# Optimization experiments

Measured on AMD Instinct MI355X. Metric: run time of the kernel, lower is better.

Reference implementation:

```python
import jax, jax.numpy as jnp
import numpy as np

B, S, D, H = 2, 2048, 1024, 16
HD = D // H  # head_dim = 64


def setup_inputs() -> dict:
    key = jax.random.key(0)
    ks = jax.random.split(key, 6)
    sc = 0.02
    return {
        "x": jax.random.normal(ks[0], (B, S, D), dtype=jnp.float32),
        "W_query": jax.random.normal(ks[1], (D, D), dtype=jnp.float32) * sc,
        "W_key": jax.random.normal(ks[2], (D, D), dtype=jnp.float32) * sc,
        "W_value": jax.random.normal(ks[3], (D, D), dtype=jnp.float32) * sc,
        "W_out": jax.random.normal(ks[4], (D, D), dtype=jnp.float32) * sc,
        "b_out": jnp.zeros((D,), dtype=jnp.float32),
    }


def reference(x, W_query, W_key, W_value, W_out, b_out):
    b, s, _ = x.shape
    # torch nn.Linear: y = x @ W.T ; split into heads [b, h, s, hd]
    def proj(W):
        return (x @ W.T).reshape(b, s, H, HD).transpose(0, 2, 1, 3)

    q, k, v = proj(W_query), proj(W_key), proj(W_value)
    scores = jnp.einsum("bhqd,bhkd->bhqk", q, k)  # [b, h, s, s]
    causal = jnp.tril(jnp.ones((s, s), dtype=bool))  # True = keep
    scores = jnp.where(causal, scores, -jnp.inf)
    weights = jax.nn.softmax(scores / np.sqrt(HD).astype(np.float32), axis=-1)
    # dropout p=0.0 -> identity
    ctx = jnp.einsum("bhqk,bhkd->bhqd", weights, v)
    ctx = ctx.transpose(0, 2, 1, 3).reshape(b, s, D)
    return ctx @ W_out.T + b_out
```

## Files before the change

kernel.cpp:

```cpp
#include <hip/hip_runtime.h>
#include <stdint.h>

#define B_  2
#define S_  2048
#define D_  1024
#define H_  16
#define HD_ 64
#define M_  (B_*S_)

typedef __attribute__((ext_vector_type(8)))  short bf16x8;
typedef __attribute__((ext_vector_type(4)))  float f32x4;
typedef __attribute__((ext_vector_type(16))) float f32x16;
typedef __attribute__((ext_vector_type(4)))  unsigned int u32x4;


__device__ __forceinline__ unsigned short f2bf(float f) {
    unsigned int u = __float_as_uint(f);
    unsigned int r = (u + 0x7fffu + ((u >> 16) & 1u)) >> 16;
    return (unsigned short)r;
}

__device__ __forceinline__ unsigned int cvt_pk_bf16(float lo, float hi) {
    unsigned int r;
    asm("v_cvt_pk_bf16_f32 %0, %1, %2" : "=v"(r) : "v"(lo), "v"(hi));
    return r;
}

__device__ __forceinline__ void gload_lds16(const void* g, void* l) {
    __builtin_amdgcn_global_load_lds(
        (const __attribute__((address_space(1))) unsigned int*)g,
        (__attribute__((address_space(3))) unsigned int*)l,
        16, 0, 0);
}


__global__ __launch_bounds__(256) void cast_all(
    const float* __restrict__ x,
    const float* __restrict__ wq, const float* __restrict__ wk,
    const float* __restrict__ wv, const float* __restrict__ wo,
    unsigned short* __restrict__ dst)
{
    int b = blockIdx.x;
    const float* src;
    size_t soff, doff;
    float sc = 1.0f;
    if (b < 2048) {
        src = x; soff = (size_t)b * 2048; doff = soff;
    } else {
        int r  = (b - 2048) >> 9;
        int lb = (b - 2048) & 511;
        src = (r == 0) ? wq : (r == 1) ? wk : (r == 2) ? wv : wo;
        if (r <= 1) sc = 0.4246609093670877f;
        soff = (size_t)lb * 2048;
        doff = (size_t)4194304 + (size_t)r * 1048576 + soff;
    }
    int idx = threadIdx.x * 8;
    float4 a = *reinterpret_cast<const float4*>(src + soff + idx);
    float4 c = *reinterpret_cast<const float4*>(src + soff + idx + 4);
    unsigned short t[8];
    t[0]=f2bf(a.x*sc); t[1]=f2bf(a.y*sc); t[2]=f2bf(a.z*sc); t[3]=f2bf(a.w*sc);
    t[4]=f2bf(c.x*sc); t[5]=f2bf(c.y*sc); t[6]=f2bf(c.z*sc); t[7]=f2bf(c.w*sc);
    *reinterpret_cast<uint4*>(dst + doff + idx) = *reinterpret_cast<const uint4*>(t);
}


template <bool BIAS, typename CT>
__global__ __launch_bounds__(256) void gemm_bt(
    const unsigned short* __restrict__ A,
    const unsigned short* __restrict__ Bm,
    CT* __restrict__ C,
    const float* __restrict__ bias,
    int M, int N, int K)
{
    constexpr int BK = 32;
    __shared__ unsigned short As[128 * BK];
    __shared__ unsigned short Bs[128 * BK];

    const int tid  = threadIdx.x;
    const int lane = tid & 63;
    const int wid  = tid >> 6;
    const int wr = wid >> 1, wc = wid & 1;
    const int l15 = lane & 15, lhi = lane >> 4;
    const int tm = blockIdx.y * 128, tn = blockIdx.x * 128;

    f32x4 acc[4][4] = {};

    const int srow = (lane >> 2);
    const int scol = (lane & 3) * 8;

    for (int k0 = 0; k0 < K; k0 += BK) {
        __syncthreads();
        #pragma unroll
        for (int i = 0; i < 2; ++i) {
            int chunk = wid * 2 + i;
            int row = chunk * 16 + srow;
            gload_lds16(A  + (size_t)(tm + row) * K + k0 + scol, (void*)(As + chunk * 512));
            gload_lds16(Bm + (size_t)(tn + row) * K + k0 + scol, (void*)(Bs + chunk * 512));
        }
        __syncthreads();

        bf16x8 af[4], bfr[4];
        #pragma unroll
        for (int i = 0; i < 4; ++i)
            af[i] = *reinterpret_cast<const bf16x8*>(As + (wr * 64 + i * 16 + l15) * BK + lhi * 8);
        #pragma unroll
        for (int j = 0; j < 4; ++j)
            bfr[j] = *reinterpret_cast<const bf16x8*>(Bs + (wc * 64 + j * 16 + l15) * BK + lhi * 8);
        #pragma unroll
        for (int i = 0; i < 4; ++i)
            #pragma unroll
            for (int j = 0; j < 4; ++j)
                acc[i][j] = __builtin_amdgcn_mfma_f32_16x16x32_bf16(af[i], bfr[j], acc[i][j], 0, 0, 0);
    }

    #pragma unroll
    for (int i = 0; i < 4; ++i) {
        #pragma unroll
        for (int j = 0; j < 4; ++j) {
            int col = tn + wc * 64 + j * 16 + l15;
            float bv = BIAS ? bias[col] : 0.0f;
            #pragma unroll
            for (int r = 0; r < 4; ++r) {
                int row = tm + wr * 64 + i * 16 + lhi * 4 + r;
                float v = acc[i][j][r] + bv;
                if constexpr (sizeof(CT) == 2) {
                    ((unsigned short*)C)[(size_t)row * N + col] = f2bf(v);
                } else {
                    ((float*)C)[(size_t)row * N + col] = v;
                }
            }
        }
    }
}


__global__ __launch_bounds__(256) void gemm_qkv(
    const unsigned short* __restrict__ A,
    const unsigned short* __restrict__ Bm,
    unsigned short* __restrict__ Cqk,
    unsigned short* __restrict__ Vt)
{
    constexpr int BK = 32, K = 1024;
    __shared__ unsigned short As[128 * BK];
    __shared__ unsigned short Bs[128 * BK];

    const int tid  = threadIdx.x;
    const int lane = tid & 63;
    const int wid  = tid >> 6;
    const int wr = wid >> 1, wc = wid & 1;
    const int l15 = lane & 15, lhi = lane >> 4;
    const int tm = blockIdx.y * 128, tn = blockIdx.x * 128;

    f32x4 acc[4][4] = {};

    const int srow = (lane >> 2);
    const int scol = (lane & 3) * 8;

    for (int k0 = 0; k0 < K; k0 += BK) {
        __syncthreads();
        #pragma unroll
        for (int i = 0; i < 2; ++i) {
            int chunk = wid * 2 + i;
            int row = chunk * 16 + srow;
            gload_lds16(A  + (size_t)(tm + row) * K + k0 + scol, (void*)(As + chunk * 512));
            gload_lds16(Bm + (size_t)(tn + row) * K + k0 + scol, (void*)(Bs + chunk * 512));
        }
        __syncthreads();

        bf16x8 af[4], bfr[4];
        #pragma unroll
        for (int i = 0; i < 4; ++i)
            af[i] = *reinterpret_cast<const bf16x8*>(As + (wr * 64 + i * 16 + l15) * BK + lhi * 8);
        #pragma unroll
        for (int j = 0; j < 4; ++j)
            bfr[j] = *reinterpret_cast<const bf16x8*>(Bs + (wc * 64 + j * 16 + l15) * BK + lhi * 8);
        #pragma unroll
        for (int i = 0; i < 4; ++i)
            #pragma unroll
            for (int j = 0; j < 4; ++j)
                acc[i][j] = __builtin_amdgcn_mfma_f32_16x16x32_bf16(af[i], bfr[j], acc[i][j], 0, 0, 0);
    }

    const bool isV = (tn >= 2048);
    #pragma unroll
    for (int i = 0; i < 4; ++i) {
        #pragma unroll
        for (int j = 0; j < 4; ++j) {
            int col = tn + wc * 64 + j * 16 + l15;
            int row0 = tm + wr * 64 + i * 16 + lhi * 4;
            if (!isV) {
                #pragma unroll
                for (int r = 0; r < 4; ++r)
                    Cqk[(size_t)(row0 + r) * 2048 + col] = f2bf(acc[i][j][r]);
            } else {
                unsigned short t[4];
                #pragma unroll
                for (int r = 0; r < 4; ++r) t[r] = f2bf(acc[i][j][r]);
                *reinterpret_cast<uint2*>(Vt + (size_t)(col - 2048) * M_ + row0) =
                    *reinterpret_cast<const uint2*>(t);
            }
        }
    }
}


__global__ __launch_bounds__(256, 4) void attn_kernel(
    const unsigned short* __restrict__ QK,
    const unsigned short* __restrict__ VT,
    unsigned short* __restrict__ Ctx)
{
    __shared__ unsigned short Ks[4][32 * 64];
    __shared__ unsigned short Vs[4][64 * 32];

    const int tid  = threadIdx.x;
    const int lane = tid & 63;
    const int wid  = tid >> 6;
    const int l31  = lane & 31;
    const int hi   = lane >> 5;

    const int lin  = blockIdx.x;
    const int idx  = lin >> 3;
    const int bh   = (lin & 7) + 8 * (idx & 3);
    const int qb   = 63 - (idx >> 2);
    const int b = bh >> 4, h = bh & 15;
    const size_t baseRow = (size_t)b * S_;
    const int qw = qb * 32;
    const int q  = qw + l31;

    bf16x8 qf[4];
    #pragma unroll
    for (int s = 0; s < 4; ++s)
        qf[s] = *reinterpret_cast<const bf16x8*>(
            QK + (baseRow + q) * 2048 + h * HD_ + s * 16 + hi * 8);

    float l = 0.0f;
    f32x16 oacc[2] = {};

    const int nkt = qb + 1;

    const int kr  = lane >> 3;
    const int ks  = lane & 7;
    const int vr  = lane >> 2;
    const int vsl = lane & 3;

#define STAGE_K(kt_) do {                                                      \
    int k0_ = (kt_) * 32;                                                      \
    _Pragma("unroll")                                                          \
    for (int i_ = 0; i_ < 4; ++i_) {                                           \
        int krow_ = i_ * 8 + kr;                                               \
        int ksc_  = (ks ^ kr) * 8;                                             \
        gload_lds16(QK + (baseRow + k0_ + krow_) * 2048 + D_ + h * HD_ + ksc_, \
                    (void*)(&Ks[wid][i_ * 512]));                              \
    } } while (0)
#define STAGE_V(kt_) do {                                                      \
    int k0_ = (kt_) * 32;                                                      \
    _Pragma("unroll")                                                          \
    for (int i_ = 0; i_ < 4; ++i_) {                                           \
        int vrow_ = i_ * 16 + vr;                                              \
        int vsc_  = (vsl ^ ((vrow_ >> 1) & 3)) * 8;                            \
        gload_lds16(VT + (size_t)(h * HD_ + vrow_) * M_ + baseRow + k0_ + vsc_,\
                    (void*)(&Vs[wid][i_ * 512]));                              \
    } } while (0)

    if (wid < nkt) {
        STAGE_K(wid);
        STAGE_V(wid);
        for (int kt = wid; kt < nkt; kt += 4) {
            const bool more = (kt + 4 < nkt);

            asm volatile("s_waitcnt vmcnt(4)" ::: "memory");
            __builtin_amdgcn_sched_barrier(0);

            const unsigned short* Kc = &Ks[wid][0];

            f32x16 sc = {};
            #pragma unroll
            for (int s = 0; s < 4; ++s) {
                int sl = (2 * s + hi) ^ (l31 & 7);
                bf16x8 kf = *reinterpret_cast<const bf16x8*>(Kc + l31 * 64 + sl * 8);
                sc = __builtin_amdgcn_mfma_f32_32x32x16_bf16(kf, qf[s], sc, 0, 0, 0);
            }

            asm volatile("s_waitcnt lgkmcnt(0)" ::: "memory");
            __builtin_amdgcn_sched_barrier(0);
            if (more) STAGE_K(kt + 4);

            if (kt == qb) {
                #pragma unroll
                for (int r = 0; r < 16; ++r) {
                    int kl = kt * 32 + (r & 3) + 8 * (r >> 2) + 4 * hi;
                    if (kl > q) sc[r] = -INFINITY;
                }
            }

            unsigned int g0, g1, g2, g3, g4, g5, g6, g7;
            float ps = 0.0f;
            {
                float e0, e1, e2, e3;
                e0=exp2f(sc[0]);  e1=exp2f(sc[1]);  e2=exp2f(sc[2]);  e3=exp2f(sc[3]);
                ps += (e0+e1)+(e2+e3); g0 = cvt_pk_bf16(e0,e1); g1 = cvt_pk_bf16(e2,e3);
                e0=exp2f(sc[4]);  e1=exp2f(sc[5]);  e2=exp2f(sc[6]);  e3=exp2f(sc[7]);
                ps += (e0+e1)+(e2+e3); g2 = cvt_pk_bf16(e0,e1); g3 = cvt_pk_bf16(e2,e3);
                e0=exp2f(sc[8]);  e1=exp2f(sc[9]);  e2=exp2f(sc[10]); e3=exp2f(sc[11]);
                ps += (e0+e1)+(e2+e3); g4 = cvt_pk_bf16(e0,e1); g5 = cvt_pk_bf16(e2,e3);
                e0=exp2f(sc[12]); e1=exp2f(sc[13]); e2=exp2f(sc[14]); e3=exp2f(sc[15]);
                ps += (e0+e1)+(e2+e3); g6 = cvt_pk_bf16(e0,e1); g7 = cvt_pk_bf16(e2,e3);
            }
            l += ps;

            asm("v_permlane32_swap_b32 %0, %1" : "+v"(g0), "+v"(g2));
            asm("v_permlane32_swap_b32 %0, %1" : "+v"(g1), "+v"(g3));
            asm("v_permlane32_swap_b32 %0, %1" : "+v"(g4), "+v"(g6));
            asm("v_permlane32_swap_b32 %0, %1" : "+v"(g5), "+v"(g7));
            bf16x8 pa0 = __builtin_bit_cast(bf16x8, (u32x4){g0, g1, g2, g3});
            bf16x8 pa1 = __builtin_bit_cast(bf16x8, (u32x4){g4, g5, g6, g7});

            if (more) asm volatile("s_waitcnt vmcnt(4)" ::: "memory");
            else      asm volatile("s_waitcnt vmcnt(0)" ::: "memory");
            __builtin_amdgcn_sched_barrier(0);

            const unsigned short* Vc = &Vs[wid][0];
            bf16x8 vf[2][2];
            #pragma unroll
            for (int dt = 0; dt < 2; ++dt)
                #pragma unroll
                for (int s = 0; s < 2; ++s) {
                    int d = dt * 32 + l31;
                    int sl = (2 * s + hi) ^ ((d >> 1) & 3);
                    vf[dt][s] = *reinterpret_cast<const bf16x8*>(Vc + d * 32 + sl * 8);
                }

            asm volatile("s_waitcnt lgkmcnt(0)" ::: "memory");
            __builtin_amdgcn_sched_barrier(0);
            if (more) STAGE_V(kt + 4);

            __builtin_amdgcn_s_setprio(1);
            #pragma unroll
            for (int dt = 0; dt < 2; ++dt) {
                oacc[dt] = __builtin_amdgcn_mfma_f32_32x32x16_bf16(pa0, vf[dt][0], oacc[dt], 0, 0, 0);
                oacc[dt] = __builtin_amdgcn_mfma_f32_32x32x16_bf16(pa1, vf[dt][1], oacc[dt], 0, 0, 0);
            }
            __builtin_amdgcn_s_setprio(0);
        }
    }
#undef STAGE_K
#undef STAGE_V

    float* Olw = (float*)&Ks[wid][0];
    float* Lpw = (float*)&Vs[wid][0];
    float lc = l + __shfl_xor(l, 32, 64);
    if (hi == 0) Lpw[l31] = lc;

    const int cq = tid >> 3;
    const int cd = (tid & 7) * 4;
    float inv = 0.0f;
    #pragma unroll
    for (int ph = 0; ph < 2; ++ph) {
        __syncthreads();
        #pragma unroll
        for (int r = 0; r < 16; ++r) {
            int qr = (r & 3) + 8 * (r >> 2) + 4 * hi;
            Olw[qr * 32 + l31] = oacc[ph][r];
        }
        __syncthreads();
        float s0 = 0, s1 = 0, s2 = 0, s3 = 0, lt = 0;
        #pragma unroll
        for (int w = 0; w < 4; ++w) {
            const float* O = (const float*)&Ks[w][0];
            f32x4 a = *reinterpret_cast<const f32x4*>(O + cq * 32 + cd);
            s0 += a[0]; s1 += a[1]; s2 += a[2]; s3 += a[3];
            if (ph == 0) lt += ((const float*)&Vs[w][0])[cq];
        }
        if (ph == 0) inv = 1.0f / lt;
        unsigned short o[4];
        o[0] = f2bf(s0 * inv); o[1] = f2bf(s1 * inv);
        o[2] = f2bf(s2 * inv); o[3] = f2bf(s3 * inv);
        *reinterpret_cast<uint2*>(
            Ctx + (baseRow + qw + cq) * D_ + h * HD_ + ph * 32 + cd) =
            *reinterpret_cast<const uint2*>(o);
    }
}


extern "C" void kernel_launch(void* const* d_in, const int* in_sizes, int n_in,
                              void* d_out, int out_size, void* d_ws, size_t ws_size,
                              hipStream_t stream) {
    const float* x  = (const float*)d_in[0];
    const float* wq = (const float*)d_in[1];
    const float* wk = (const float*)d_in[2];
    const float* wv = (const float*)d_in[3];
    const float* wo = (const float*)d_in[4];
    const float* bo = (const float*)d_in[5];

    unsigned short* ws = (unsigned short*)d_ws;
    unsigned short* xb  = ws;
    unsigned short* wqb = xb  + 4194304;
    unsigned short* wob = wqb + 3145728;
    unsigned short* QKb = wob + 1048576;
    unsigned short* VT  = QKb + 8388608;
    unsigned short* Cx  = VT  + 4194304;

    cast_all<<<4096, 256, 0, stream>>>(x, wq, wk, wv, wo, xb);

    gemm_qkv<<<dim3(24, 32), 256, 0, stream>>>(xb, wqb, QKb, VT);

    attn_kernel<<<2048, 256, 0, stream>>>(QKb, VT, Cx);

    gemm_bt<true, float><<<dim3(8, 32), 256, 0, stream>>>(
        Cx, wob, (float*)d_out, bo, M_, D_, D_);
}
```

Before: 109.1 us.

## Pair causal query tiles per attention block and narrow output GEMM tiles

The attention kernel now gives each block two query tiles, a short one (pidx) and a long one (63-pidx). Each pair of waves splits that tile's key range across two waves instead of four, so per-block causal work is balanced and the grid shrinks from 2048 to 1024 blocks. The reduction epilogue combines only the two waves that belong to the same query tile and writes 16-byte stores. The output projection becomes a dedicated 128x64-tile GEMM with a 512-block grid, replacing the 128x128 generic one that used only 256 blocks. This fills more CUs, at the cost of less reuse per block and longer serial key loops per wave.

```diff
diff --git a/kernel.cpp b/kernel.cpp
--- a/kernel.cpp
+++ b/kernel.cpp
@@ -64,76 +64,6 @@
 }
 
 
-template <bool BIAS, typename CT>
-__global__ __launch_bounds__(256) void gemm_bt(
-    const unsigned short* __restrict__ A,
-    const unsigned short* __restrict__ Bm,
-    CT* __restrict__ C,
-    const float* __restrict__ bias,
-    int M, int N, int K)
-{
-    constexpr int BK = 32;
-    __shared__ unsigned short As[128 * BK];
-    __shared__ unsigned short Bs[128 * BK];
-
-    const int tid  = threadIdx.x;
-    const int lane = tid & 63;
-    const int wid  = tid >> 6;
-    const int wr = wid >> 1, wc = wid & 1;
-    const int l15 = lane & 15, lhi = lane >> 4;
-    const int tm = blockIdx.y * 128, tn = blockIdx.x * 128;
-
-    f32x4 acc[4][4] = {};
-
-    const int srow = (lane >> 2);
-    const int scol = (lane & 3) * 8;
-
-    for (int k0 = 0; k0 < K; k0 += BK) {
-        __syncthreads();
-        #pragma unroll
-        for (int i = 0; i < 2; ++i) {
-            int chunk = wid * 2 + i;
-            int row = chunk * 16 + srow;
-            gload_lds16(A  + (size_t)(tm + row) * K + k0 + scol, (void*)(As + chunk * 512));
-            gload_lds16(Bm + (size_t)(tn + row) * K + k0 + scol, (void*)(Bs + chunk * 512));
-        }
-        __syncthreads();
-
-        bf16x8 af[4], bfr[4];
-        #pragma unroll
-        for (int i = 0; i < 4; ++i)
-            af[i] = *reinterpret_cast<const bf16x8*>(As + (wr * 64 + i * 16 + l15) * BK + lhi * 8);
-        #pragma unroll
-        for (int j = 0; j < 4; ++j)
-            bfr[j] = *reinterpret_cast<const bf16x8*>(Bs + (wc * 64 + j * 16 + l15) * BK + lhi * 8);
-        #pragma unroll
-        for (int i = 0; i < 4; ++i)
-            #pragma unroll
-            for (int j = 0; j < 4; ++j)
-                acc[i][j] = __builtin_amdgcn_mfma_f32_16x16x32_bf16(af[i], bfr[j], acc[i][j], 0, 0, 0);
-    }
-
-    #pragma unroll
-    for (int i = 0; i < 4; ++i) {
-        #pragma unroll
-        for (int j = 0; j < 4; ++j) {
-            int col = tn + wc * 64 + j * 16 + l15;
-            float bv = BIAS ? bias[col] : 0.0f;
-            #pragma unroll
-            for (int r = 0; r < 4; ++r) {
-                int row = tm + wr * 64 + i * 16 + lhi * 4 + r;
-                float v = acc[i][j][r] + bv;
-                if constexpr (sizeof(CT) == 2) {
-                    ((unsigned short*)C)[(size_t)row * N + col] = f2bf(v);
-                } else {
-                    ((float*)C)[(size_t)row * N + col] = v;
-                }
-            }
-        }
-    }
-}
-
-
 __global__ __launch_bounds__(256) void gemm_qkv(
     const unsigned short* __restrict__ A,
     const unsigned short* __restrict__ Bm,
@@ -204,6 +134,69 @@
 }
 
 
+__global__ __launch_bounds__(256) void gemm_out(
+    const unsigned short* __restrict__ A,
+    const unsigned short* __restrict__ Bm,
+    float* __restrict__ C,
+    const float* __restrict__ bias)
+{
+    constexpr int BK = 32, K = 1024, N = 1024;
+    __shared__ unsigned short As[128 * BK];
+    __shared__ unsigned short Bs[64 * BK];
+
+    const int tid  = threadIdx.x;
+    const int lane = tid & 63;
+    const int wid  = tid >> 6;
+    const int wr = wid >> 1, wc = wid & 1;
+    const int l15 = lane & 15, lhi = lane >> 4;
+    const int tm = blockIdx.y * 128, tn = blockIdx.x * 64;
+
+    f32x4 acc[4][2] = {};
+
+    const int srow = (lane >> 2);
+    const int scol = (lane & 3) * 8;
+
+    for (int k0 = 0; k0 < K; k0 += BK) {
+        __syncthreads();
+        #pragma unroll
+        for (int i = 0; i < 2; ++i) {
+            int chunk = wid * 2 + i;
+            int row = chunk * 16 + srow;
+            gload_lds16(A + (size_t)(tm + row) * K + k0 + scol, (void*)(As + chunk * 512));
+        }
+        gload_lds16(Bm + (size_t)(tn + wid * 16 + srow) * K + k0 + scol, (void*)(Bs + wid * 512));
+        __syncthreads();
+
+        bf16x8 af[4], bfr[2];
+        #pragma unroll
+        for (int i = 0; i < 4; ++i)
+            af[i] = *reinterpret_cast<const bf16x8*>(As + (wr * 64 + i * 16 + l15) * BK + lhi * 8);
+        #pragma unroll
+        for (int j = 0; j < 2; ++j)
+            bfr[j] = *reinterpret_cast<const bf16x8*>(Bs + (wc * 32 + j * 16 + l15) * BK + lhi * 8);
+        #pragma unroll
+        for (int i = 0; i < 4; ++i)
+            #pragma unroll
+            for (int j = 0; j < 2; ++j)
+                acc[i][j] = __builtin_amdgcn_mfma_f32_16x16x32_bf16(af[i], bfr[j], acc[i][j], 0, 0, 0);
+    }
+
+    #pragma unroll
+    for (int i = 0; i < 4; ++i) {
+        #pragma unroll
+        for (int j = 0; j < 2; ++j) {
+            int col = tn + wc * 32 + j * 16 + l15;
+            float bv = bias[col];
+            #pragma unroll
+            for (int r = 0; r < 4; ++r) {
+                int row = tm + wr * 64 + i * 16 + lhi * 4 + r;
+                C[(size_t)row * N + col] = acc[i][j][r] + bv;
+            }
+        }
+    }
+}
+
+
 __global__ __launch_bounds__(256, 4) void attn_kernel(
     const unsigned short* __restrict__ QK,
     const unsigned short* __restrict__ VT,
@@ -217,11 +210,14 @@
     const int wid  = tid >> 6;
     const int l31  = lane & 31;
     const int hi   = lane >> 5;
+    const int pw   = wid >> 1;
+    const int sw   = wid & 1;
 
     const int lin  = blockIdx.x;
     const int idx  = lin >> 3;
     const int bh   = (lin & 7) + 8 * (idx & 3);
-    const int qb   = 63 - (idx >> 2);
+    const int pidx = idx >> 2;
+    const int qb   = pw ? (63 - pidx) : pidx;
     const int b = bh >> 4, h = bh & 15;
     const size_t baseRow = (size_t)b * S_;
     const int qw = qb * 32;
@@ -235,8 +231,6 @@
 
     float l = 0.0f;
     f32x16 oacc[2] = {};
-
-    const int nkt = qb + 1;
 
     const int kr  = lane >> 3;
     const int ks  = lane & 7;
@@ -262,11 +256,11 @@
                     (void*)(&Vs[wid][i_ * 512]));                              \
     } } while (0)
 
-    if (wid < nkt) {
-        STAGE_K(wid);
-        STAGE_V(wid);
-        for (int kt = wid; kt < nkt; kt += 4) {
-            const bool more = (kt + 4 < nkt);
+    if (sw <= qb) {
+        STAGE_K(sw);
+        STAGE_V(sw);
+        for (int kt = sw; kt <= qb; kt += 2) {
+            const bool more = (kt + 2 <= qb);
 
             asm volatile("s_waitcnt vmcnt(4)" ::: "memory");
             __builtin_amdgcn_sched_barrier(0);
@@ -283,7 +277,7 @@
 
             asm volatile("s_waitcnt lgkmcnt(0)" ::: "memory");
             __builtin_amdgcn_sched_barrier(0);
-            if (more) STAGE_K(kt + 4);
+            if (more) STAGE_K(kt + 2);
 
             if (kt == qb) {
                 #pragma unroll
@@ -332,7 +326,7 @@
 
             asm volatile("s_waitcnt lgkmcnt(0)" ::: "memory");
             __builtin_amdgcn_sched_barrier(0);
-            if (more) STAGE_V(kt + 4);
+            if (more) STAGE_V(kt + 2);
 
             __builtin_amdgcn_s_setprio(1);
             #pragma unroll
@@ -351,8 +345,11 @@
     float lc = l + __shfl_xor(l, 32, 64);
     if (hi == 0) Lpw[l31] = lc;
 
-    const int cq = tid >> 3;
-    const int cd = (tid & 7) * 4;
+    const int p  = tid >> 7;
+    const int t  = tid & 127;
+    const int cq = t >> 2;
+    const int cd = (t & 3) * 8;
+    const int qwp = (p ? (63 - pidx) : pidx) * 32;
     float inv = 0.0f;
     #pragma unroll
     for (int ph = 0; ph < 2; ++ph) {
@@ -363,21 +360,25 @@
             Olw[qr * 32 + l31] = oacc[ph][r];
         }
         __syncthreads();
-        float s0 = 0, s1 = 0, s2 = 0, s3 = 0, lt = 0;
-        #pragma unroll
-        for (int w = 0; w < 4; ++w) {
+        float s0 = 0, s1 = 0, s2 = 0, s3 = 0;
+        float s4 = 0, s5 = 0, s6 = 0, s7 = 0;
+        float lt = 0;
+        #pragma unroll
+        for (int w = 2 * p; w < 2 * p + 2; ++w) {
             const float* O = (const float*)&Ks[w][0];
             f32x4 a = *reinterpret_cast<const f32x4*>(O + cq * 32 + cd);
+            f32x4 c = *reinterpret_cast<const f32x4*>(O + cq * 32 + cd + 4);
             s0 += a[0]; s1 += a[1]; s2 += a[2]; s3 += a[3];
+            s4 += c[0]; s5 += c[1]; s6 += c[2]; s7 += c[3];
             if (ph == 0) lt += ((const float*)&Vs[w][0])[cq];
         }
         if (ph == 0) inv = 1.0f / lt;
-        unsigned short o[4];
-        o[0] = f2bf(s0 * inv); o[1] = f2bf(s1 * inv);
-        o[2] = f2bf(s2 * inv); o[3] = f2bf(s3 * inv);
-        *reinterpret_cast<uint2*>(
-            Ctx + (baseRow + qw + cq) * D_ + h * HD_ + ph * 32 + cd) =
-            *reinterpret_cast<const uint2*>(o);
+        unsigned short o[8];
+        o[0]=f2bf(s0*inv); o[1]=f2bf(s1*inv); o[2]=f2bf(s2*inv); o[3]=f2bf(s3*inv);
+        o[4]=f2bf(s4*inv); o[5]=f2bf(s5*inv); o[6]=f2bf(s6*inv); o[7]=f2bf(s7*inv);
+        *reinterpret_cast<uint4*>(
+            Ctx + (baseRow + qwp + cq) * D_ + h * HD_ + ph * 32 + cd) =
+            *reinterpret_cast<const uint4*>(o);
     }
 }
 
@@ -404,8 +405,7 @@
 
     gemm_qkv<<<dim3(24, 32), 256, 0, stream>>>(xb, wqb, QKb, VT);
 
-    attn_kernel<<<2048, 256, 0, stream>>>(QKb, VT, Cx);
-
-    gemm_bt<true, float><<<dim3(8, 32), 256, 0, stream>>>(
-        Cx, wob, (float*)d_out, bo, M_, D_, D_);
-}
+    attn_kernel<<<1024, 256, 0, stream>>>(QKb, VT, Cx);
+
+    gemm_out<<<dim3(16, 32), 256, 0, stream>>>(Cx, wob, (float*)d_out, bo);
+}
```

Result: faster. 106.9 us (-2.0%).
